# Performance work log

Hardware: AMD Instinct MI355X
Metric: run time of the kernel (lower is better)

Reference implementation:

```python
import jax, jax.numpy as jnp
import numpy as np

N, K, C, HID, G = 100000, 16, 64, 16, 128  # points, knn, channels, mlp hidden, voxel grid


def setup_inputs() -> dict:
    key = jax.random.key(0)
    ks = jax.random.split(key, 8)
    x_F = jax.random.normal(ks[0], (N, C), dtype=jnp.float32)
    idx = jax.random.randint(ks[1], (N, K), 0, N)  # knn neighbor indices

    # --- synthetic unique voxel coords + 3x3x3 sparse-conv neighbor map ---
    rng = np.random.default_rng(0)
    lin = rng.choice(G ** 3, size=N, replace=False)
    lut = np.full(G ** 3, -1, dtype=np.int64)
    lut[lin] = np.arange(N)
    xc, yc, zc = lin // (G * G), (lin // G) % G, lin % G
    nbrs = []
    for dx in (-1, 0, 1):
        for dy in (-1, 0, 1):
            for dz in (-1, 0, 1):
                nx, ny, nz = xc + dx, yc + dy, zc + dz
                valid = (nx >= 0) & (nx < G) & (ny >= 0) & (ny < G) & (nz >= 0) & (nz < G)
                nlin = np.clip(nx, 0, G - 1) * G * G + np.clip(ny, 0, G - 1) * G + np.clip(nz, 0, G - 1)
                nbrs.append(np.where(valid, lut[nlin], -1))
    conv_idx = jnp.asarray(np.stack(nbrs, axis=1))  # (N, 27), -1 = no neighbor voxel

    # --- learned params: shared channel MLP + sparse conv3d(2->1, k=3) weight ---
    W1 = jax.random.normal(ks[2], (C, HID), dtype=jnp.float32) / np.sqrt(C)
    b1 = jnp.zeros((HID,), dtype=jnp.float32)
    W2 = jax.random.normal(ks[3], (HID, C), dtype=jnp.float32) / np.sqrt(HID)
    b2 = jnp.zeros((C,), dtype=jnp.float32)
    conv_w = jax.random.normal(ks[4], (27, 2, 1), dtype=jnp.float32) / np.sqrt(27 * 2)
    return {"x_F": x_F, "W1": W1, "b1": b1, "W2": W2, "b2": b2,
            "conv_w": conv_w, "idx": idx, "conv_idx": conv_idx}


def reference(x_F, W1, b1, W2, b2, conv_w, idx, conv_idx):
    n = x_F.shape[0]

    def mlp(v):
        return jax.nn.relu(v @ W1 + b1) @ W2 + b2

    # channel attention: knn gather -> mean/max pool over k -> shared MLP gate
    g = x_F[idx]                                           # (n, k, c)
    gate = jax.nn.sigmoid(mlp(g.mean(axis=1)) + mlp(g.max(axis=1)))
    outse = x_F * gate                                     # (n, c)

    # spatial attention: pool over flattened (k*c), sparse conv3d(2->1)
    g2 = outse[idx].reshape(n, -1)                         # (n, k*c)
    z = jnp.stack([g2.mean(axis=1), g2.max(axis=1)], axis=1)  # (n, 2)
    mask = (conv_idx >= 0).astype(z.dtype)[..., None]      # (n, 27, 1)
    zn = z[jnp.clip(conv_idx, 0)] * mask                   # (n, 27, 2)
    convf = jnp.einsum('nkc,kco->no', zn, conv_w)          # (n, 1)
    return outse * jax.nn.sigmoid(convf)
```

## Files before the change

### kernel.cpp

```cpp
#include <hip/hip_runtime.h>
#include <math.h>

#define KNN 16
#define CH 64
#define HID 16
#define NEG_BIG (-3.402823466e+38f)

__device__ __forceinline__ float sigmoidf_(float x) {
    return 1.0f / (1.0f + __expf(-x));
}

__device__ __forceinline__ float fold16(float v[HID], int sub) {
    #pragma unroll
    for (int m = 8; m >= 1; m >>= 1) {
        bool hi = (sub & m) != 0;
        #pragma unroll
        for (int i = 0; i < m; ++i) {
            float s    = hi ? v[i] : v[i + m];
            float keep = hi ? v[i + m] : v[i];
            v[i] = keep + __shfl_xor(s, m);
        }
    }
    return v[0];
}

__global__ __launch_bounds__(256, 4) void kA(const float4* __restrict__ xv,
        const float* __restrict__ W1, const float* __restrict__ b1,
        const float* __restrict__ W2, const float* __restrict__ b2,
        const int* __restrict__ idx,
        float4* __restrict__ outse, float2* __restrict__ rowstat, int n) {
    __shared__ float4 w1q[256];
    __shared__ float4 w2q[256];
    int t = threadIdx.x;
    {
        int h = t >> 4, s = t & 15;
        float4 a;
        a.x = W1[(4 * s + 0) * HID + h];
        a.y = W1[(4 * s + 1) * HID + h];
        a.z = W1[(4 * s + 2) * HID + h];
        a.w = W1[(4 * s + 3) * HID + h];
        w1q[t] = a;
        w2q[t] = ((const float4*)W2)[t];
    }
    __syncthreads();

    int p = blockIdx.x * 16 + (t >> 4);
    int sub = t & 15;
    if (p >= n) return;

    int jj = idx[p * KNN + sub];
    int jall[KNN];
    #pragma unroll
    for (int k = 0; k < KNN; ++k) jall[k] = __shfl(jj, k, 16);

    float4 vbuf[KNN];
    #pragma unroll
    for (int k = 0; k < KNN; ++k) vbuf[k] = xv[jall[k] * 16 + sub];
    float4 own = xv[p * 16 + sub];
    float bb = b1[sub];
    float4 bq = ((const float4*)b2)[sub];

    float4 sum = vbuf[0];
    float4 mx  = vbuf[0];
    #pragma unroll
    for (int k = 1; k < KNN; ++k) {
        float4 v = vbuf[k];
        sum.x += v.x; sum.y += v.y; sum.z += v.z; sum.w += v.w;
        mx.x = fmaxf(mx.x, v.x); mx.y = fmaxf(mx.y, v.y);
        mx.z = fmaxf(mx.z, v.z); mx.w = fmaxf(mx.w, v.w);
    }
    const float inv_k = 1.0f / KNN;
    float4 mean = {sum.x * inv_k, sum.y * inv_k, sum.z * inv_k, sum.w * inv_k};

    float Hm, Hx;
    {
        float pm[HID];
        #pragma unroll
        for (int h = 0; h < HID; ++h) {
            float4 w = w1q[h * 16 + sub];
            pm[h] = mean.x * w.x + mean.y * w.y + mean.z * w.z + mean.w * w.w;
        }
        Hm = fold16(pm, sub);
    }
    {
        float px[HID];
        #pragma unroll
        for (int h = 0; h < HID; ++h) {
            float4 w = w1q[h * 16 + sub];
            px[h] = mx.x * w.x + mx.y * w.y + mx.z * w.z + mx.w * w.w;
        }
        Hx = fold16(px, sub);
    }
    float H = fmaxf(Hm + bb, 0.0f) + fmaxf(Hx + bb, 0.0f);

    float4 acc = {0.f, 0.f, 0.f, 0.f};
    #pragma unroll
    for (int h = 0; h < HID; ++h) {
        float Hh = __shfl(H, h, 16);
        float4 w = w2q[h * 16 + sub];
        acc.x += Hh * w.x; acc.y += Hh * w.y; acc.z += Hh * w.z; acc.w += Hh * w.w;
    }
    float4 o;
    o.x = own.x * sigmoidf_(acc.x + 2.0f * bq.x);
    o.y = own.y * sigmoidf_(acc.y + 2.0f * bq.y);
    o.z = own.z * sigmoidf_(acc.z + 2.0f * bq.z);
    o.w = own.w * sigmoidf_(acc.w + 2.0f * bq.w);
    outse[p * 16 + sub] = o;

    float sm = o.x + o.y + o.z + o.w;
    float sx = fmaxf(fmaxf(o.x, o.y), fmaxf(o.z, o.w));
    #pragma unroll
    for (int m = 8; m >= 1; m >>= 1) {
        sm += __shfl_xor(sm, m);
        sx = fmaxf(sx, __shfl_xor(sx, m));
    }
    if (sub == 0) rowstat[p] = make_float2(sm * (1.0f / 64.0f), sx);
}

__global__ __launch_bounds__(256) void kB(const int4* __restrict__ idxv,
        const float2* __restrict__ rowstat, float2* __restrict__ z, int n) {
    int i = blockIdx.x * 256 + threadIdx.x;
    if (i >= n) return;
    float zm = 0.0f, zx = NEG_BIG;
    #pragma unroll
    for (int q = 0; q < 4; ++q) {
        int4 jj = idxv[i * 4 + q];
        float2 s0 = rowstat[jj.x];
        float2 s1 = rowstat[jj.y];
        float2 s2 = rowstat[jj.z];
        float2 s3 = rowstat[jj.w];
        zm += s0.x + s1.x + s2.x + s3.x;
        zx = fmaxf(zx, fmaxf(fmaxf(s0.y, s1.y), fmaxf(s2.y, s3.y)));
    }
    z[i] = make_float2(zm * (1.0f / 16.0f), zx);
}

__global__ __launch_bounds__(256) void kC1(const int* __restrict__ conv_idx,
        const float* __restrict__ conv_w, const float2* __restrict__ z,
        float* __restrict__ sig, int n) {
    __shared__ float cw[54];
    if (threadIdx.x < 54) cw[threadIdx.x] = conv_w[threadIdx.x];
    __syncthreads();
    int i = blockIdx.x * 256 + threadIdx.x;
    if (i >= n) return;
    float acc = 0.0f;
    #pragma unroll
    for (int k = 0; k < 27; ++k) {
        int j = conv_idx[i * 27 + k];
        if (j >= 0) {
            float2 zz = z[j];
            acc += zz.x * cw[2 * k] + zz.y * cw[2 * k + 1];
        }
    }
    sig[i] = sigmoidf_(acc);
}

__global__ __launch_bounds__(256) void kC2(const float4* __restrict__ outse,
        const float* __restrict__ sig, float4* __restrict__ out, int n4) {
    int i = blockIdx.x * 256 + threadIdx.x;
    if (i >= n4) return;
    float s = sig[i >> 4];
    float4 v = outse[i];
    out[i] = make_float4(v.x * s, v.y * s, v.z * s, v.w * s);
}

extern "C" void kernel_launch(void* const* d_in, const int* in_sizes, int n_in,
                              void* d_out, int out_size, void* d_ws, size_t ws_size,
                              hipStream_t stream) {
    const float* x_F    = (const float*)d_in[0];
    const float* W1     = (const float*)d_in[1];
    const float* b1     = (const float*)d_in[2];
    const float* W2     = (const float*)d_in[3];
    const float* b2     = (const float*)d_in[4];
    const float* conv_w = (const float*)d_in[5];
    const int*   idx    = (const int*)d_in[6];
    const int*   cidx   = (const int*)d_in[7];
    int n = in_sizes[0] / CH;

    char* ws = (char*)d_ws;
    float*  outse   = (float*)ws;
    float2* rowstat = (float2*)(ws + (size_t)n * CH * 4);
    float2* zz      = (float2*)(ws + (size_t)n * CH * 4 + (size_t)n * 8);
    float*  sig     = (float*)(ws + (size_t)n * CH * 4 + (size_t)n * 16);

    int blkA = (n + 15) / 16;
    kA<<<blkA, 256, 0, stream>>>((const float4*)x_F, W1, b1, W2, b2, idx,
                                 (float4*)outse, rowstat, n);
    int blkP = (n + 255) / 256;
    kB<<<blkP, 256, 0, stream>>>((const int4*)idx, rowstat, zz, n);
    kC1<<<blkP, 256, 0, stream>>>(cidx, conv_w, zz, sig, n);
    int n4 = n * (CH / 4);
    int blkE = (n4 + 255) / 256;
    kC2<<<blkE, 256, 0, stream>>>((const float4*)outse, sig, (float4*)d_out, n4);
}
```

Measured before the change: 200.4 us.

## Stage kNN gathers through LDS via global_load_lds and fuse conv gate with scaling

The channel-attention kernel now gathers neighbour feature rows straight into shared memory with async global-to-LDS loads, in two batches of eight, instead of holding sixteen float4 registers per thread. This is meant to cut register pressure and raise occupancy. The trade-off is fewer loads in flight per wave, plus hand-written waitcnt encodings and LDS reuse that depend on subtle ordering. Separately, the sparse-conv sigmoid kernel and the final scaling kernel are merged into one launch with the gate held in shared memory. This removes the sig buffer round trip and one launch, and the conv mask is now applied without a branch.

```diff
diff --git a/kernel.cpp b/kernel.cpp
--- a/kernel.cpp
+++ b/kernel.cpp
@@ -27,10 +27,12 @@
 __global__ __launch_bounds__(256, 4) void kA(const float4* __restrict__ xv,
         const float* __restrict__ W1, const float* __restrict__ b1,
         const float* __restrict__ W2, const float* __restrict__ b2,
-        const int* __restrict__ idx,
+        const int4* __restrict__ idxv,
         float4* __restrict__ outse, float2* __restrict__ rowstat, int n) {
     __shared__ float4 w1q[256];
     __shared__ float4 w2q[256];
+    __shared__ float4 stage[4][8][64];
+
     int t = threadIdx.x;
     {
         int h = t >> 4, s = t & 15;
@@ -46,29 +48,55 @@
 
     int p = blockIdx.x * 16 + (t >> 4);
     int sub = t & 15;
+    int w = t >> 6;
+    int lane = t & 63;
     if (p >= n) return;
 
-    int jj = idx[p * KNN + sub];
-    int jall[KNN];
-    #pragma unroll
-    for (int k = 0; k < KNN; ++k) jall[k] = __shfl(jj, k, 16);
-
-    float4 vbuf[KNN];
-    #pragma unroll
-    for (int k = 0; k < KNN; ++k) vbuf[k] = xv[jall[k] * 16 + sub];
+    int4 ja0 = idxv[p * 4 + 0];
+    int4 jb0 = idxv[p * 4 + 1];
+    int4 ja1 = idxv[p * 4 + 2];
+    int4 jb1 = idxv[p * 4 + 3];
+
+    auto issue = [&](int j, int k) {
+        __builtin_amdgcn_global_load_lds(
+            (const __attribute__((address_space(1))) void*)(xv + ((size_t)j * 16 + sub)),
+            (__attribute__((address_space(3))) void*)(&stage[w][k][0]),
+            16, 0, 0);
+    };
+
+    issue(ja0.x, 0); issue(ja0.y, 1); issue(ja0.z, 2); issue(ja0.w, 3);
+    issue(jb0.x, 4); issue(jb0.y, 5); issue(jb0.z, 6); issue(jb0.w, 7);
     float4 own = xv[p * 16 + sub];
     float bb = b1[sub];
     float4 bq = ((const float4*)b2)[sub];
 
-    float4 sum = vbuf[0];
-    float4 mx  = vbuf[0];
-    #pragma unroll
-    for (int k = 1; k < KNN; ++k) {
-        float4 v = vbuf[k];
+    __builtin_amdgcn_s_waitcnt(0x0F70);
+
+    float4 sum, mx;
+    {
+        float4 v = stage[w][0][lane];
+        sum = v; mx = v;
+    }
+    #pragma unroll
+    for (int k = 1; k < 8; ++k) {
+        float4 v = stage[w][k][lane];
         sum.x += v.x; sum.y += v.y; sum.z += v.z; sum.w += v.w;
         mx.x = fmaxf(mx.x, v.x); mx.y = fmaxf(mx.y, v.y);
         mx.z = fmaxf(mx.z, v.z); mx.w = fmaxf(mx.w, v.w);
     }
+
+    issue(ja1.x, 0); issue(ja1.y, 1); issue(ja1.z, 2); issue(ja1.w, 3);
+    issue(jb1.x, 4); issue(jb1.y, 5); issue(jb1.z, 6); issue(jb1.w, 7);
+    __builtin_amdgcn_s_waitcnt(0x0F70);
+
+    #pragma unroll
+    for (int k = 0; k < 8; ++k) {
+        float4 v = stage[w][k][lane];
+        sum.x += v.x; sum.y += v.y; sum.z += v.z; sum.w += v.w;
+        mx.x = fmaxf(mx.x, v.x); mx.y = fmaxf(mx.y, v.y);
+        mx.z = fmaxf(mx.z, v.z); mx.w = fmaxf(mx.w, v.w);
+    }
+
     const float inv_k = 1.0f / KNN;
     float4 mean = {sum.x * inv_k, sum.y * inv_k, sum.z * inv_k, sum.w * inv_k};
 
@@ -77,8 +105,8 @@
         float pm[HID];
         #pragma unroll
         for (int h = 0; h < HID; ++h) {
-            float4 w = w1q[h * 16 + sub];
-            pm[h] = mean.x * w.x + mean.y * w.y + mean.z * w.z + mean.w * w.w;
+            float4 wv = w1q[h * 16 + sub];
+            pm[h] = mean.x * wv.x + mean.y * wv.y + mean.z * wv.z + mean.w * wv.w;
         }
         Hm = fold16(pm, sub);
     }
@@ -86,8 +114,8 @@
         float px[HID];
         #pragma unroll
         for (int h = 0; h < HID; ++h) {
-            float4 w = w1q[h * 16 + sub];
-            px[h] = mx.x * w.x + mx.y * w.y + mx.z * w.z + mx.w * w.w;
+            float4 wv = w1q[h * 16 + sub];
+            px[h] = mx.x * wv.x + mx.y * wv.y + mx.z * wv.z + mx.w * wv.w;
         }
         Hx = fold16(px, sub);
     }
@@ -97,8 +125,8 @@
     #pragma unroll
     for (int h = 0; h < HID; ++h) {
         float Hh = __shfl(H, h, 16);
-        float4 w = w2q[h * 16 + sub];
-        acc.x += Hh * w.x; acc.y += Hh * w.y; acc.z += Hh * w.z; acc.w += Hh * w.w;
+        float4 wv = w2q[h * 16 + sub];
+        acc.x += Hh * wv.x; acc.y += Hh * wv.y; acc.z += Hh * wv.z; acc.w += Hh * wv.w;
     }
     float4 o;
     o.x = own.x * sigmoidf_(acc.x + 2.0f * bq.x);
@@ -135,33 +163,36 @@
     z[i] = make_float2(zm * (1.0f / 16.0f), zx);
 }
 
-__global__ __launch_bounds__(256) void kC1(const int* __restrict__ conv_idx,
+__global__ __launch_bounds__(256) void kC(const int* __restrict__ conv_idx,
         const float* __restrict__ conv_w, const float2* __restrict__ z,
-        float* __restrict__ sig, int n) {
+        const float4* __restrict__ outse, float4* __restrict__ out, int n) {
     __shared__ float cw[54];
+    __shared__ float sgate[256];
     if (threadIdx.x < 54) cw[threadIdx.x] = conv_w[threadIdx.x];
     __syncthreads();
-    int i = blockIdx.x * 256 + threadIdx.x;
-    if (i >= n) return;
-    float acc = 0.0f;
-    #pragma unroll
-    for (int k = 0; k < 27; ++k) {
-        int j = conv_idx[i * 27 + k];
-        if (j >= 0) {
-            float2 zz = z[j];
-            acc += zz.x * cw[2 * k] + zz.y * cw[2 * k + 1];
-        }
-    }
-    sig[i] = sigmoidf_(acc);
-}
-
-__global__ __launch_bounds__(256) void kC2(const float4* __restrict__ outse,
-        const float* __restrict__ sig, float4* __restrict__ out, int n4) {
-    int i = blockIdx.x * 256 + threadIdx.x;
-    if (i >= n4) return;
-    float s = sig[i >> 4];
-    float4 v = outse[i];
-    out[i] = make_float4(v.x * s, v.y * s, v.z * s, v.w * s);
+    int base = blockIdx.x * 256;
+    int i = base + threadIdx.x;
+    if (i < n) {
+        float acc = 0.0f;
+        #pragma unroll
+        for (int k = 0; k < 27; ++k) {
+            int j = conv_idx[i * 27 + k];
+            int jc = j >= 0 ? j : 0;
+            float msk = j >= 0 ? 1.0f : 0.0f;
+            float2 zz = z[jc];
+            acc += msk * (zz.x * cw[2 * k] + zz.y * cw[2 * k + 1]);
+        }
+        sgate[threadIdx.x] = sigmoidf_(acc);
+    }
+    __syncthreads();
+    int npts = n - base; if (npts > 256) npts = 256;
+    int tot = npts * 16;
+    for (int q = threadIdx.x; q < tot; q += 256) {
+        float s = sgate[q >> 4];
+        float4 v = outse[(size_t)base * 16 + q];
+        float4 r = make_float4(v.x * s, v.y * s, v.z * s, v.w * s);
+        out[(size_t)base * 16 + q] = r;
+    }
 }
 
 extern "C" void kernel_launch(void* const* d_in, const int* in_sizes, int n_in,
@@ -181,15 +212,12 @@
     float*  outse   = (float*)ws;
     float2* rowstat = (float2*)(ws + (size_t)n * CH * 4);
     float2* zz      = (float2*)(ws + (size_t)n * CH * 4 + (size_t)n * 8);
-    float*  sig     = (float*)(ws + (size_t)n * CH * 4 + (size_t)n * 16);
 
     int blkA = (n + 15) / 16;
-    kA<<<blkA, 256, 0, stream>>>((const float4*)x_F, W1, b1, W2, b2, idx,
-                                 (float4*)outse, rowstat, n);
+    kA<<<blkA, 256, 0, stream>>>((const float4*)x_F, W1, b1, W2, b2,
+                                 (const int4*)idx, (float4*)outse, rowstat, n);
     int blkP = (n + 255) / 256;
     kB<<<blkP, 256, 0, stream>>>((const int4*)idx, rowstat, zz, n);
-    kC1<<<blkP, 256, 0, stream>>>(cidx, conv_w, zz, sig, n);
-    int n4 = n * (CH / 4);
-    int blkE = (n4 + 255) / 256;
-    kC2<<<blkE, 256, 0, stream>>>((const float4*)outse, sig, (float4*)d_out, n4);
-}
+    kC<<<blkP, 256, 0, stream>>>(cidx, conv_w, zz, (const float4*)outse,
+                                 (float4*)d_out, n);
+}
```

Result: slower. 286.4 us (+42.9%).
